# Optimization experiments

Measured on AMD Instinct MI355X. Metric: run time of the kernel, lower is better.

## Reference

```python
import jax, jax.numpy as jnp
import numpy as np
from jax import lax

B, T, I, H = 128, 512, 300, 256


def setup_inputs() -> dict:
    key = jax.random.key(0)
    ks = jax.random.split(key, 10)
    k = 1.0 / np.sqrt(H)
    u = lambda kk, shape: jax.random.uniform(kk, shape, jnp.float32, -k, k)
    return {
        "x": jax.random.normal(ks[0], (B, T, I), jnp.float32),
        "W_ih_f": u(ks[1], (4 * H, I)),
        "W_hh_f": u(ks[2], (4 * H, H)),
        "b_f": u(ks[3], (4 * H,)),
        "W_ih_b": u(ks[4], (4 * H, I)),
        "W_hh_b": u(ks[5], (4 * H, H)),
        "b_b": u(ks[6], (4 * H,)),
        "W_lin": u(ks[7], (2, 2 * H)),
        "b_lin": u(ks[8], (2,)),
    }


def _lstm_dir(x, W_ih, W_hh, b, reverse):
    # Precompute input projections for all timesteps: [B, T, 4H]
    xp = jnp.einsum("bti,gi->btg", x, W_ih) + b
    if reverse:
        xp = xp[:, ::-1]
    h0 = jnp.zeros((x.shape[0], H), x.dtype)
    c0 = jnp.zeros((x.shape[0], H), x.dtype)

    def step(carry, xt):
        h, c = carry
        g = xt + h @ W_hh.T  # [B, 4H]
        i_g, f_g, g_g, o_g = jnp.split(g, 4, axis=-1)  # torch gate order i,f,g,o
        i_g = jax.nn.sigmoid(i_g)
        f_g = jax.nn.sigmoid(f_g)
        g_g = jnp.tanh(g_g)
        o_g = jax.nn.sigmoid(o_g)
        c = f_g * c + i_g * g_g
        h = o_g * jnp.tanh(c)
        return (h, c), h

    _, hs = lax.scan(step, (h0, c0), jnp.swapaxes(xp, 0, 1))  # [T, B, H]
    hs = jnp.swapaxes(hs, 0, 1)  # [B, T, H]
    if reverse:
        hs = hs[:, ::-1]
    return hs


def reference(x, W_ih_f, W_hh_f, b_f, W_ih_b, W_hh_b, b_b, W_lin, b_lin):
    hf = _lstm_dir(x, W_ih_f, W_hh_f, b_f, reverse=False)  # [B, T, H]
    hb = _lstm_dir(x, W_ih_b, W_hh_b, b_b, reverse=True)   # [B, T, H]
    last = jnp.concatenate([hf[:, -1], hb[:, -1]], axis=-1)  # [B, 2H]
    return last @ W_lin.T + b_lin  # [B, 2]
```

## Files before the change

### kernel.cpp

```cpp
#include <hip/hip_runtime.h>
#include <cstdint>
#include <cstddef>

typedef _Float16 half2v __attribute__((ext_vector_type(2)));
typedef _Float16 half4v __attribute__((ext_vector_type(4)));
typedef _Float16 half8v __attribute__((ext_vector_type(8)));
typedef float f32x4 __attribute__((ext_vector_type(4)));

#if __has_builtin(__builtin_amdgcn_fdot2)
#define FDOT2(a, b, c) __builtin_amdgcn_fdot2((a), (b), (c), false)
#else
static __device__ __forceinline__ float fdot2_fb(half2v a, half2v b, float c) {
    return c + (float)a[0] * (float)b[0] + (float)a[1] * (float)b[1];
}
#define FDOT2(a, b, c) fdot2_fb((a), (b), (c))
#endif

__device__ __forceinline__ float sigm(float x) { return 1.0f / (1.0f + __expf(-x)); }
__device__ __forceinline__ float tanh_(float x) { return 1.0f - 2.0f / (__expf(2.0f * x) + 1.0f); }

#define BB 128
#define TT 512
#define II 300
#define HH 256
#define GG 1024

__global__ __launch_bounds__(256, 3) void gemm_xp(
    const float* __restrict__ X, const float* __restrict__ W,
    const float* __restrict__ bias, _Float16* __restrict__ XP)
{
    __shared__ _Float16 As[128 * 32];
    __shared__ _Float16 Bs[128 * 32];

    const int t = threadIdx.x;
    const int m0 = blockIdx.y * 128;
    const int n0 = blockIdx.x * 128;
    const int kpos = t & 7;
    const int rbase = t >> 3;
    const int lane = t & 63;
    const int wv = t >> 6;
    const int mq = (wv >> 1) * 4;
    const int nq = (wv & 1) * 4;

    f32x4 acc[4][4];
#pragma unroll
    for (int i = 0; i < 4; ++i)
#pragma unroll
        for (int j = 0; j < 4; ++j) acc[i][j] = f32x4{0.f, 0.f, 0.f, 0.f};

    for (int kc = 0; kc < 320; kc += 32) {
        __syncthreads();
        const int k0 = kc + kpos * 4;
#pragma unroll
        for (int rr = 0; rr < 4; ++rr) {
            const int row = rbase + rr * 32;
            float4 va = {0.f, 0.f, 0.f, 0.f}, vb = {0.f, 0.f, 0.f, 0.f};
            if (k0 < 300) {
                va = *(const float4*)(X + (size_t)(m0 + row) * II + k0);
                vb = *(const float4*)(W + (size_t)(n0 + row) * II + k0);
            }
            const int idx = (row >> 4) * 512 + (kpos >> 1) * 128 + (row & 15) * 8 + (kpos & 1) * 4;
            half4v ha = {(_Float16)va.x, (_Float16)va.y, (_Float16)va.z, (_Float16)va.w};
            half4v hb = {(_Float16)vb.x, (_Float16)vb.y, (_Float16)vb.z, (_Float16)vb.w};
            *(half4v*)(&As[idx]) = ha;
            *(half4v*)(&Bs[idx]) = hb;
        }
        __syncthreads();

        half8v af[4], bf[4];
#pragma unroll
        for (int i = 0; i < 4; ++i) {
            af[i] = *(const half8v*)(&As[(mq + i) * 512 + (lane >> 4) * 128 + (lane & 15) * 8]);
            bf[i] = *(const half8v*)(&Bs[(nq + i) * 512 + (lane >> 4) * 128 + (lane & 15) * 8]);
        }
#pragma unroll
        for (int i = 0; i < 4; ++i)
#pragma unroll
            for (int j = 0; j < 4; ++j)
                acc[i][j] = __builtin_amdgcn_mfma_f32_16x16x32_f16(af[i], bf[j], acc[i][j], 0, 0, 0);
    }

#pragma unroll
    for (int j = 0; j < 4; ++j) {
        const int n = n0 + (nq + j) * 16 + (lane & 15);
        const float bv = bias[n];
#pragma unroll
        for (int i = 0; i < 4; ++i) {
#pragma unroll
            for (int r = 0; r < 4; ++r) {
                const int m = m0 + (mq + i) * 16 + (lane >> 4) * 4 + r;
                XP[(size_t)m * GG + n] = (_Float16)(acc[i][j][r] + bv);
            }
        }
    }
}

__global__ __launch_bounds__(512, 2) void lstm_fwd(
    const float* __restrict__ Whh, const _Float16* __restrict__ XP,
    float* __restrict__ HF)
{
    __shared__ _Float16 wlds[5 * GG * 8];
    __shared__ float glds[GG];
    __shared__ __align__(16) _Float16 hlds[HH];

    const int t = threadIdx.x;
    const int b = blockIdx.x;
    const int j1 = t + 512;

    half2v w0[108], w1[108];
#pragma unroll
    for (int i = 0; i < 54; ++i) {
        float4 v = *(const float4*)(Whh + (size_t)t * HH + i * 4);
        w0[2 * i] = half2v{(_Float16)v.x, (_Float16)v.y};
        w0[2 * i + 1] = half2v{(_Float16)v.z, (_Float16)v.w};
    }
#pragma unroll
    for (int i = 0; i < 54; ++i) {
        float4 v = *(const float4*)(Whh + (size_t)j1 * HH + i * 4);
        w1[2 * i] = half2v{(_Float16)v.x, (_Float16)v.y};
        w1[2 * i + 1] = half2v{(_Float16)v.z, (_Float16)v.w};
    }
#pragma unroll
    for (int grp = 0; grp < 5; ++grp) {
        float4 a = *(const float4*)(Whh + (size_t)t * HH + 216 + grp * 8);
        float4 c4 = *(const float4*)(Whh + (size_t)t * HH + 216 + grp * 8 + 4);
        half8v hv = {(_Float16)a.x, (_Float16)a.y, (_Float16)a.z, (_Float16)a.w,
                     (_Float16)c4.x, (_Float16)c4.y, (_Float16)c4.z, (_Float16)c4.w};
        *(half8v*)(&wlds[grp * (GG * 8) + t * 8]) = hv;
        float4 a2 = *(const float4*)(Whh + (size_t)j1 * HH + 216 + grp * 8);
        float4 c2 = *(const float4*)(Whh + (size_t)j1 * HH + 216 + grp * 8 + 4);
        half8v hv2 = {(_Float16)a2.x, (_Float16)a2.y, (_Float16)a2.z, (_Float16)a2.w,
                      (_Float16)c2.x, (_Float16)c2.y, (_Float16)c2.z, (_Float16)c2.w};
        *(half8v*)(&wlds[grp * (GG * 8) + j1 * 8]) = hv2;
    }
    if (t < HH) hlds[t] = (_Float16)0.f;
    float c = 0.0f;
    __syncthreads();

    const _Float16* xp_b = XP + (size_t)b * TT * GG;
    for (int ts = 0; ts < TT; ++ts) {
        const _Float16 x0 = xp_b[(size_t)ts * GG + t];
        const _Float16 x1 = xp_b[(size_t)ts * GG + j1];
        float a0 = 0.f, a1 = 0.f;
#pragma unroll
        for (int cq = 0; cq < 27; ++cq) {
            half8v hv = *(const half8v*)(&hlds[cq * 8]);
#pragma unroll
            for (int w = 0; w < 4; ++w) {
                half2v hp = {hv[2 * w], hv[2 * w + 1]};
                a0 = FDOT2(hp, w0[cq * 4 + w], a0);
                a1 = FDOT2(hp, w1[cq * 4 + w], a1);
            }
        }
#pragma unroll
        for (int grp = 0; grp < 5; ++grp) {
            half8v hv = *(const half8v*)(&hlds[216 + grp * 8]);
            half8v wa = *(const half8v*)(&wlds[grp * (GG * 8) + t * 8]);
            half8v wb = *(const half8v*)(&wlds[grp * (GG * 8) + j1 * 8]);
#pragma unroll
            for (int w = 0; w < 4; ++w) {
                half2v hp = {hv[2 * w], hv[2 * w + 1]};
                half2v wap = {wa[2 * w], wa[2 * w + 1]};
                half2v wbp = {wb[2 * w], wb[2 * w + 1]};
                a0 = FDOT2(hp, wap, a0);
                a1 = FDOT2(hp, wbp, a1);
            }
        }
        a0 += (float)x0;
        a1 += (float)x1;
        glds[t] = a0;
        glds[j1] = a1;
        __syncthreads();
        if (t < HH) {
            const float gi = glds[t];
            const float gf = glds[t + 256];
            const float gg = glds[t + 512];
            const float go = glds[t + 768];
            c = sigm(gf) * c + sigm(gi) * tanh_(gg);
            const float h = sigm(go) * tanh_(c);
            hlds[t] = (_Float16)h;
            if (ts == TT - 1) HF[(size_t)b * HH + t] = h;
        }
        __syncthreads();
    }
}

__global__ __launch_bounds__(256) void lstm_bwd(
    const float* __restrict__ X, const float* __restrict__ Wih,
    const float* __restrict__ bb, float* __restrict__ HB)
{
    __shared__ float xs[II];
    const int b = blockIdx.x, t = threadIdx.x;
    const float* xrow = X + ((size_t)b * TT + (TT - 1)) * II;
    if (t < 75) *(float4*)(&xs[t * 4]) = *(const float4*)(xrow + t * 4);
    __syncthreads();
    if (t < HH) {
        float ai = 0.f, ag = 0.f, ao = 0.f;
        const float4* wi = (const float4*)(Wih + (size_t)t * II);
        const float4* wg = (const float4*)(Wih + (size_t)(t + 512) * II);
        const float4* wo = (const float4*)(Wih + (size_t)(t + 768) * II);
        for (int k4 = 0; k4 < 75; ++k4) {
            float4 xv = *(const float4*)(&xs[k4 * 4]);
            float4 a = wi[k4], g4 = wg[k4], o4 = wo[k4];
            ai += xv.x * a.x + xv.y * a.y + xv.z * a.z + xv.w * a.w;
            ag += xv.x * g4.x + xv.y * g4.y + xv.z * g4.z + xv.w * g4.w;
            ao += xv.x * o4.x + xv.y * o4.y + xv.z * o4.z + xv.w * o4.w;
        }
        ai += bb[t];
        ag += bb[t + 512];
        ao += bb[t + 768];
        const float cg = sigm(ai) * tanh_(ag);
        HB[(size_t)b * HH + t] = sigm(ao) * tanh_(cg);
    }
}

__global__ __launch_bounds__(256) void final_k(
    const float* __restrict__ HF, const float* __restrict__ HB,
    const float* __restrict__ Wlin, const float* __restrict__ blin,
    float* __restrict__ OUT)
{
    const int t = threadIdx.x;
    const int b = t >> 1, jj = t & 1;
    float acc = blin[jj];
    const float* wf = Wlin + jj * 512;
    const float* wb = Wlin + jj * 512 + 256;
    const float* hf = HF + (size_t)b * HH;
    const float* hb = HB + (size_t)b * HH;
    for (int k = 0; k < HH; k += 4) {
        float4 h4 = *(const float4*)(hf + k);
        float4 w4 = *(const float4*)(wf + k);
        float4 g4 = *(const float4*)(hb + k);
        float4 v4 = *(const float4*)(wb + k);
        acc += h4.x * w4.x + h4.y * w4.y + h4.z * w4.z + h4.w * w4.w;
        acc += g4.x * v4.x + g4.y * v4.y + g4.z * v4.z + g4.w * v4.w;
    }
    OUT[b * 2 + jj] = acc;
}

extern "C" void kernel_launch(void* const* d_in, const int* in_sizes, int n_in,
                              void* d_out, int out_size, void* d_ws, size_t ws_size,
                              hipStream_t stream)
{
    const float* x = (const float*)d_in[0];
    const float* Wihf = (const float*)d_in[1];
    const float* Whhf = (const float*)d_in[2];
    const float* bf = (const float*)d_in[3];
    const float* Wihb = (const float*)d_in[4];
    const float* Whhb = (const float*)d_in[5];
    const float* bbv = (const float*)d_in[6];
    const float* Wlin = (const float*)d_in[7];
    const float* blin = (const float*)d_in[8];
    float* out = (float*)d_out;
    (void)Whhb; (void)in_sizes; (void)n_in; (void)out_size; (void)ws_size;

    _Float16* xp = (_Float16*)d_ws;
    float* hf = (float*)((char*)d_ws + (size_t)BB * TT * GG * 2);
    float* hb = hf + (size_t)BB * HH;

    lstm_bwd<<<BB, 256, 0, stream>>>(x, Wihb, bbv, hb);
    gemm_xp<<<dim3(GG / 128, (BB * TT) / 128), 256, 0, stream>>>(x, Wihf, bf, xp);
    lstm_fwd<<<BB, 512, 0, stream>>>(Whhf, xp, hf);
    final_k<<<1, 256, 0, stream>>>(hf, hb, Wlin, blin, out);
}
```

Measured before the change: 1.348 ms.

## Rebalance LSTM recurrent weights between registers and LDS, prefetch next-step projections

Moves more of the recurrent weight matrix from registers into shared memory (192 columns in registers, 64 in LDS instead of 216/40), which lowers register pressure. The input projection for the next timestep is now loaded one iteration ahead, so its global-memory latency overlaps the current step's dot products. The gate nonlinearity is computed redundantly by all 512 threads using partner values read from LDS, which removes the idle-thread branch around that math. In exchange, each step issues more LDS weight reads and does duplicated transcendental work.

```diff
diff --git a/kernel.cpp b/kernel.cpp
--- a/kernel.cpp
+++ b/kernel.cpp
@@ -99,89 +99,111 @@
     const float* __restrict__ Whh, const _Float16* __restrict__ XP,
     float* __restrict__ HF)
 {
-    __shared__ _Float16 wlds[5 * GG * 8];
+    __shared__ _Float16 wlds[8 * GG * 8];
     __shared__ float glds[GG];
     __shared__ __align__(16) _Float16 hlds[HH];
 
     const int t = threadIdx.x;
     const int b = blockIdx.x;
-    const int j1 = t + 512;
-
-    half2v w0[108], w1[108];
-#pragma unroll
-    for (int i = 0; i < 54; ++i) {
+    const int r1 = t + 512;
+
+    half2v w0[96], w1[96];
+#pragma unroll
+    for (int i = 0; i < 48; ++i) {
         float4 v = *(const float4*)(Whh + (size_t)t * HH + i * 4);
-        w0[2 * i] = half2v{(_Float16)v.x, (_Float16)v.y};
+        w0[2 * i]     = half2v{(_Float16)v.x, (_Float16)v.y};
         w0[2 * i + 1] = half2v{(_Float16)v.z, (_Float16)v.w};
     }
 #pragma unroll
-    for (int i = 0; i < 54; ++i) {
-        float4 v = *(const float4*)(Whh + (size_t)j1 * HH + i * 4);
-        w1[2 * i] = half2v{(_Float16)v.x, (_Float16)v.y};
+    for (int i = 0; i < 48; ++i) {
+        float4 v = *(const float4*)(Whh + (size_t)r1 * HH + i * 4);
+        w1[2 * i]     = half2v{(_Float16)v.x, (_Float16)v.y};
         w1[2 * i + 1] = half2v{(_Float16)v.z, (_Float16)v.w};
     }
 #pragma unroll
-    for (int grp = 0; grp < 5; ++grp) {
-        float4 a = *(const float4*)(Whh + (size_t)t * HH + 216 + grp * 8);
-        float4 c4 = *(const float4*)(Whh + (size_t)t * HH + 216 + grp * 8 + 4);
+    for (int grp = 0; grp < 8; ++grp) {
+        float4 a  = *(const float4*)(Whh + (size_t)t * HH + 192 + grp * 8);
+        float4 c4 = *(const float4*)(Whh + (size_t)t * HH + 192 + grp * 8 + 4);
         half8v hv = {(_Float16)a.x, (_Float16)a.y, (_Float16)a.z, (_Float16)a.w,
                      (_Float16)c4.x, (_Float16)c4.y, (_Float16)c4.z, (_Float16)c4.w};
         *(half8v*)(&wlds[grp * (GG * 8) + t * 8]) = hv;
-        float4 a2 = *(const float4*)(Whh + (size_t)j1 * HH + 216 + grp * 8);
-        float4 c2 = *(const float4*)(Whh + (size_t)j1 * HH + 216 + grp * 8 + 4);
+        float4 a2 = *(const float4*)(Whh + (size_t)r1 * HH + 192 + grp * 8);
+        float4 c2 = *(const float4*)(Whh + (size_t)r1 * HH + 192 + grp * 8 + 4);
         half8v hv2 = {(_Float16)a2.x, (_Float16)a2.y, (_Float16)a2.z, (_Float16)a2.w,
                       (_Float16)c2.x, (_Float16)c2.y, (_Float16)c2.z, (_Float16)c2.w};
-        *(half8v*)(&wlds[grp * (GG * 8) + j1 * 8]) = hv2;
+        *(half8v*)(&wlds[grp * (GG * 8) + r1 * 8]) = hv2;
     }
     if (t < HH) hlds[t] = (_Float16)0.f;
     float c = 0.0f;
     __syncthreads();
 
     const _Float16* xp_b = XP + (size_t)b * TT * GG;
+    _Float16 x0 = xp_b[t];
+    _Float16 x1 = xp_b[r1];
+
     for (int ts = 0; ts < TT; ++ts) {
-        const _Float16 x0 = xp_b[(size_t)ts * GG + t];
-        const _Float16 x1 = xp_b[(size_t)ts * GG + j1];
+        const _Float16* xp_n = xp_b + ((ts < TT - 1) ? GG : 0);
+        const _Float16 nx0 = xp_n[t];
+        const _Float16 nx1 = xp_n[r1];
+
         float a0 = 0.f, a1 = 0.f;
 #pragma unroll
-        for (int cq = 0; cq < 27; ++cq) {
+        for (int cq = 0; cq < 24; ++cq) {
             half8v hv = *(const half8v*)(&hlds[cq * 8]);
-#pragma unroll
-            for (int w = 0; w < 4; ++w) {
-                half2v hp = {hv[2 * w], hv[2 * w + 1]};
-                a0 = FDOT2(hp, w0[cq * 4 + w], a0);
-                a1 = FDOT2(hp, w1[cq * 4 + w], a1);
-            }
-        }
-#pragma unroll
-        for (int grp = 0; grp < 5; ++grp) {
-            half8v hv = *(const half8v*)(&hlds[216 + grp * 8]);
+            half2v h0 = __builtin_shufflevector(hv, hv, 0, 1);
+            half2v h1 = __builtin_shufflevector(hv, hv, 2, 3);
+            half2v h2 = __builtin_shufflevector(hv, hv, 4, 5);
+            half2v h3 = __builtin_shufflevector(hv, hv, 6, 7);
+            a0 = FDOT2(h0, w0[cq * 4 + 0], a0);
+            a1 = FDOT2(h0, w1[cq * 4 + 0], a1);
+            a0 = FDOT2(h1, w0[cq * 4 + 1], a0);
+            a1 = FDOT2(h1, w1[cq * 4 + 1], a1);
+            a0 = FDOT2(h2, w0[cq * 4 + 2], a0);
+            a1 = FDOT2(h2, w1[cq * 4 + 2], a1);
+            a0 = FDOT2(h3, w0[cq * 4 + 3], a0);
+            a1 = FDOT2(h3, w1[cq * 4 + 3], a1);
+        }
+#define LDS_W_STEP(W_IDX, I0, I1)                                          \
+        {                                                                  \
+            half2v hp  = __builtin_shufflevector(hv, hv, I0, I1);          \
+            half2v wap = __builtin_shufflevector(wa, wa, I0, I1);          \
+            half2v wbp = __builtin_shufflevector(wb, wb, I0, I1);          \
+            a0 = FDOT2(hp, wap, a0);                                       \
+            a1 = FDOT2(hp, wbp, a1);                                       \
+        }
+#pragma unroll
+        for (int grp = 0; grp < 8; ++grp) {
+            half8v hv = *(const half8v*)(&hlds[192 + grp * 8]);
             half8v wa = *(const half8v*)(&wlds[grp * (GG * 8) + t * 8]);
-            half8v wb = *(const half8v*)(&wlds[grp * (GG * 8) + j1 * 8]);
-#pragma unroll
-            for (int w = 0; w < 4; ++w) {
-                half2v hp = {hv[2 * w], hv[2 * w + 1]};
-                half2v wap = {wa[2 * w], wa[2 * w + 1]};
-                half2v wbp = {wb[2 * w], wb[2 * w + 1]};
-                a0 = FDOT2(hp, wap, a0);
-                a1 = FDOT2(hp, wbp, a1);
-            }
-        }
-        a0 += (float)x0;
-        a1 += (float)x1;
-        glds[t] = a0;
-        glds[j1] = a1;
-        __syncthreads();
+            half8v wb = *(const half8v*)(&wlds[grp * (GG * 8) + r1 * 8]);
+            LDS_W_STEP(0, 0, 1)
+            LDS_W_STEP(1, 2, 3)
+            LDS_W_STEP(2, 4, 5)
+            LDS_W_STEP(3, 6, 7)
+        }
+#undef LDS_W_STEP
+        const float o0 = a0 + (float)x0;
+        const float o1 = a1 + (float)x1;
+        glds[t] = o0;
+        glds[t + 512] = o1;
+        __syncthreads();
+        const float p0 = glds[t ^ 256];
+        const float p1 = glds[(t ^ 256) + 512];
+        const float gi = (t < 256) ? o0 : p0;
+        const float gg = (t < 256) ? o1 : p1;
+        const float gf = (t < 256) ? p0 : o0;
+        const float go = (t < 256) ? p1 : o1;
+        c = sigm(gf) * c + sigm(gi) * tanh_(gg);
+        const float h = sigm(go) * tanh_(c);
         if (t < HH) {
-            const float gi = glds[t];
-            const float gf = glds[t + 256];
-            const float gg = glds[t + 512];
-            const float go = glds[t + 768];
-            c = sigm(gf) * c + sigm(gi) * tanh_(gg);
-            const float h = sigm(go) * tanh_(c);
             hlds[t] = (_Float16)h;
             if (ts == TT - 1) HF[(size_t)b * HH + t] = h;
         }
         __syncthreads();
+
+        x0 = nx0;
+        x1 = nx1;
+        xp_b = xp_n;
     }
 }
 
```

After: 1.360 ms. About the same (+0.8%).

## Restructure LSTM recurrence: one gate row per thread, wave-local gate exchange, double-buffered h

Applied to the files above, without the earlier changes.

The recurrent kernel now runs 1024 threads per batch row, one W_hh row per thread. Rows are assigned so that the four gates of a hidden unit sit in the same wavefront, which lets the gate values be exchanged with lane shuffles instead of a shared-memory gate buffer. That removes one of the two block barriers per timestep. The hidden state is double-buffered in LDS and broadcast through readlane. The next timestep's input projection is prefetched one step ahead. The cost is fewer resident weights per thread in registers, a larger LDS weight tail, and heavy register pressure at 1024 threads, which could cause spills.

```diff
diff --git a/kernel.cpp b/kernel.cpp
--- a/kernel.cpp
+++ b/kernel.cpp
@@ -15,6 +15,10 @@
 }
 #define FDOT2(a, b, c) fdot2_fb((a), (b), (c))
 #endif
+
+__device__ __forceinline__ half2v u2h2(unsigned u) {
+    union { unsigned u; half2v h; } x; x.u = u; return x.h;
+}
 
 __device__ __forceinline__ float sigm(float x) { return 1.0f / (1.0f + __expf(-x)); }
 __device__ __forceinline__ float tanh_(float x) { return 1.0f - 2.0f / (__expf(2.0f * x) + 1.0f); }
@@ -95,93 +99,90 @@
     }
 }
 
-__global__ __launch_bounds__(512, 2) void lstm_fwd(
+__global__ __launch_bounds__(1024) void lstm_fwd(
     const float* __restrict__ Whh, const _Float16* __restrict__ XP,
     float* __restrict__ HF)
 {
-    __shared__ _Float16 wlds[5 * GG * 8];
-    __shared__ float glds[GG];
-    __shared__ __align__(16) _Float16 hlds[HH];
+    __shared__ _Float16 wlds[8][1024 * 8];
+    __shared__ __align__(16) _Float16 hlds[2][HH];
 
     const int t = threadIdx.x;
     const int b = blockIdx.x;
-    const int j1 = t + 512;
-
-    half2v w0[108], w1[108];
-#pragma unroll
-    for (int i = 0; i < 54; ++i) {
-        float4 v = *(const float4*)(Whh + (size_t)t * HH + i * 4);
-        w0[2 * i] = half2v{(_Float16)v.x, (_Float16)v.y};
-        w0[2 * i + 1] = half2v{(_Float16)v.z, (_Float16)v.w};
-    }
-#pragma unroll
-    for (int i = 0; i < 54; ++i) {
-        float4 v = *(const float4*)(Whh + (size_t)j1 * HH + i * 4);
-        w1[2 * i] = half2v{(_Float16)v.x, (_Float16)v.y};
-        w1[2 * i + 1] = half2v{(_Float16)v.z, (_Float16)v.w};
-    }
-#pragma unroll
-    for (int grp = 0; grp < 5; ++grp) {
-        float4 a = *(const float4*)(Whh + (size_t)t * HH + 216 + grp * 8);
-        float4 c4 = *(const float4*)(Whh + (size_t)t * HH + 216 + grp * 8 + 4);
-        half8v hv = {(_Float16)a.x, (_Float16)a.y, (_Float16)a.z, (_Float16)a.w,
-                     (_Float16)c4.x, (_Float16)c4.y, (_Float16)c4.z, (_Float16)c4.w};
-        *(half8v*)(&wlds[grp * (GG * 8) + t * 8]) = hv;
-        float4 a2 = *(const float4*)(Whh + (size_t)j1 * HH + 216 + grp * 8);
-        float4 c2 = *(const float4*)(Whh + (size_t)j1 * HH + 216 + grp * 8 + 4);
-        half8v hv2 = {(_Float16)a2.x, (_Float16)a2.y, (_Float16)a2.z, (_Float16)a2.w,
-                      (_Float16)c2.x, (_Float16)c2.y, (_Float16)c2.z, (_Float16)c2.w};
-        *(half8v*)(&wlds[grp * (GG * 8) + j1 * 8]) = hv2;
-    }
-    if (t < HH) hlds[t] = (_Float16)0.f;
+    const int l = t & 63;
+    const int w = t >> 6;
+    const int v = l >> 4;
+    const int j = w * 16 + (l & 15);
+    const int row = v * 256 + j;
+
+    half2v wr[96];
+#pragma unroll
+    for (int i = 0; i < 48; ++i) {
+        float4 f = *(const float4*)(Whh + (size_t)row * HH + i * 4);
+        wr[2 * i]     = half2v{(_Float16)f.x, (_Float16)f.y};
+        wr[2 * i + 1] = half2v{(_Float16)f.z, (_Float16)f.w};
+    }
+#pragma unroll
+    for (int g = 0; g < 8; ++g) {
+        float4 fa = *(const float4*)(Whh + (size_t)row * HH + 192 + g * 8);
+        float4 fb = *(const float4*)(Whh + (size_t)row * HH + 192 + g * 8 + 4);
+        half8v hv = {(_Float16)fa.x, (_Float16)fa.y, (_Float16)fa.z, (_Float16)fa.w,
+                     (_Float16)fb.x, (_Float16)fb.y, (_Float16)fb.z, (_Float16)fb.w};
+        *(half8v*)(&wlds[g][row * 8]) = hv;
+    }
+    if (t < HH) hlds[0][t] = (_Float16)0.f;
     float c = 0.0f;
     __syncthreads();
 
-    const _Float16* xp_b = XP + (size_t)b * TT * GG;
+    const _Float16* xrow = XP + (size_t)b * TT * GG + row;
+    _Float16 xc = xrow[0];
+
     for (int ts = 0; ts < TT; ++ts) {
-        const _Float16 x0 = xp_b[(size_t)ts * GG + t];
-        const _Float16 x1 = xp_b[(size_t)ts * GG + j1];
-        float a0 = 0.f, a1 = 0.f;
-#pragma unroll
-        for (int cq = 0; cq < 27; ++cq) {
-            half8v hv = *(const half8v*)(&hlds[cq * 8]);
-#pragma unroll
-            for (int w = 0; w < 4; ++w) {
-                half2v hp = {hv[2 * w], hv[2 * w + 1]};
-                a0 = FDOT2(hp, w0[cq * 4 + w], a0);
-                a1 = FDOT2(hp, w1[cq * 4 + w], a1);
-            }
-        }
-#pragma unroll
-        for (int grp = 0; grp < 5; ++grp) {
-            half8v hv = *(const half8v*)(&hlds[216 + grp * 8]);
-            half8v wa = *(const half8v*)(&wlds[grp * (GG * 8) + t * 8]);
-            half8v wb = *(const half8v*)(&wlds[grp * (GG * 8) + j1 * 8]);
-#pragma unroll
-            for (int w = 0; w < 4; ++w) {
-                half2v hp = {hv[2 * w], hv[2 * w + 1]};
-                half2v wap = {wa[2 * w], wa[2 * w + 1]};
-                half2v wbp = {wb[2 * w], wb[2 * w + 1]};
-                a0 = FDOT2(hp, wap, a0);
-                a1 = FDOT2(hp, wbp, a1);
-            }
-        }
-        a0 += (float)x0;
-        a1 += (float)x1;
-        glds[t] = a0;
-        glds[j1] = a1;
+        const int p = ts & 1;
+        const uint4 hq = *(const uint4*)(&hlds[p][(l & 31) * 8]);
+        const _Float16 xn = xrow[(size_t)((ts < TT - 1) ? ts + 1 : ts) * GG];
+
+        float a = 0.f;
+#pragma unroll
+        for (int cq = 0; cq < 24; ++cq) {
+            const unsigned s0 = __builtin_amdgcn_readlane(hq.x, cq);
+            const unsigned s1 = __builtin_amdgcn_readlane(hq.y, cq);
+            const unsigned s2 = __builtin_amdgcn_readlane(hq.z, cq);
+            const unsigned s3 = __builtin_amdgcn_readlane(hq.w, cq);
+            a = FDOT2(u2h2(s0), wr[cq * 4 + 0], a);
+            a = FDOT2(u2h2(s1), wr[cq * 4 + 1], a);
+            a = FDOT2(u2h2(s2), wr[cq * 4 + 2], a);
+            a = FDOT2(u2h2(s3), wr[cq * 4 + 3], a);
+        }
+#pragma unroll
+        for (int g = 0; g < 8; ++g) {
+            const int cq = 24 + g;
+            half8v wv = *(const half8v*)(&wlds[g][row * 8]);
+            const unsigned s0 = __builtin_amdgcn_readlane(hq.x, cq);
+            const unsigned s1 = __builtin_amdgcn_readlane(hq.y, cq);
+            const unsigned s2 = __builtin_amdgcn_readlane(hq.z, cq);
+            const unsigned s3 = __builtin_amdgcn_readlane(hq.w, cq);
+            a = FDOT2(u2h2(s0), __builtin_shufflevector(wv, wv, 0, 1), a);
+            a = FDOT2(u2h2(s1), __builtin_shufflevector(wv, wv, 2, 3), a);
+            a = FDOT2(u2h2(s2), __builtin_shufflevector(wv, wv, 4, 5), a);
+            a = FDOT2(u2h2(s3), __builtin_shufflevector(wv, wv, 6, 7), a);
+        }
+        a += (float)xc;
+
+        const float q1 = __shfl_xor(a, 16, 64);
+        const float q2 = __shfl_xor(a, 32, 64);
+        const float q3 = __shfl_xor(a, 48, 64);
+        const float ai = (v == 0) ? a  : (v == 1) ? q1 : (v == 2) ? q2 : q3;
+        const float af = (v == 0) ? q1 : (v == 1) ? a  : (v == 2) ? q3 : q2;
+        const float ag = (v == 0) ? q2 : (v == 1) ? q3 : (v == 2) ? a  : q1;
+        const float ao = (v == 0) ? q3 : (v == 1) ? q2 : (v == 2) ? q1 : a;
+        c = sigm(af) * c + sigm(ai) * tanh_(ag);
+        const float h = sigm(ao) * tanh_(c);
+        if (v == 0) {
+            hlds[p ^ 1][j] = (_Float16)h;
+            if (ts == TT - 1) HF[(size_t)b * HH + j] = h;
+        }
         __syncthreads();
-        if (t < HH) {
-            const float gi = glds[t];
-            const float gf = glds[t + 256];
-            const float gg = glds[t + 512];
-            const float go = glds[t + 768];
-            c = sigm(gf) * c + sigm(gi) * tanh_(gg);
-            const float h = sigm(go) * tanh_(c);
-            hlds[t] = (_Float16)h;
-            if (ts == TT - 1) HF[(size_t)b * HH + t] = h;
-        }
-        __syncthreads();
+        xc = xn;
     }
 }
 
@@ -259,6 +260,6 @@
 
     lstm_bwd<<<BB, 256, 0, stream>>>(x, Wihb, bbv, hb);
     gemm_xp<<<dim3(GG / 128, (BB * TT) / 128), 256, 0, stream>>>(x, Wihf, bf, xp);
-    lstm_fwd<<<BB, 512, 0, stream>>>(Whhf, xp, hf);
+    lstm_fwd<<<BB, 1024, 0, stream>>>(Whhf, xp, hf);
     final_k<<<1, 256, 0, stream>>>(hf, hb, Wlin, blin, out);
 }
```

Result: slower. 1.818 ms (+34.9%).
